# Kernel optimization log

Hardware: AMD Instinct MI355X
Metric: run time of the kernel (lower is better)

The kernel has to match this reference:

```python
import jax, jax.numpy as jnp
import numpy as np

EMBED_DIM = 1024
WINDOW = 256
NUM_HEADS = 16
HEAD_DIM = EMBED_DIM // NUM_HEADS
SCALE = HEAD_DIM ** (-0.5)


def setup_inputs() -> dict:
    key = jax.random.key(0)
    ks = jax.random.split(key, 9)
    B, S, E = 4, 4096, EMBED_DIM
    std = E ** (-0.5)
    x = jax.random.normal(ks[0], (B, S, E), dtype=jnp.float32)
    Wq = jax.random.normal(ks[1], (E, E), dtype=jnp.float32) * std
    Wk = jax.random.normal(ks[2], (E, E), dtype=jnp.float32) * std
    Wv = jax.random.normal(ks[3], (E, E), dtype=jnp.float32) * std
    Wo = jax.random.normal(ks[4], (E, E), dtype=jnp.float32) * std
    bq = jax.random.normal(ks[5], (E,), dtype=jnp.float32) * 0.01
    bk = jax.random.normal(ks[6], (E,), dtype=jnp.float32) * 0.01
    bv = jax.random.normal(ks[7], (E,), dtype=jnp.float32) * 0.01
    bo = jax.random.normal(ks[8], (E,), dtype=jnp.float32) * 0.01
    return {"x": x, "Wq": Wq, "bq": bq, "Wk": Wk, "bk": bk,
            "Wv": Wv, "bv": bv, "Wo": Wo, "bo": bo}


def reference(x, Wq, bq, Wk, bk, Wv, bv, Wo, bo):
    B, S, E = x.shape
    W = WINDOW
    nw = S // W  # seq_len chosen divisible by window_size
    # projections (torch Linear: x @ W.T + b); no head split in the original
    q = x @ Wq.T + bq
    k = x @ Wk.T + bk
    v = x @ Wv.T + bv
    # split into non-overlapping windows: [B, nw, W, E]
    qw = q.reshape(B, nw, W, E)
    kw = k.reshape(B, nw, W, E)
    vw = v.reshape(B, nw, W, E)
    scores = jnp.einsum('bnqe,bnke->bnqk', qw, kw) * SCALE  # [B, nw, W, W]
    causal = jnp.tril(jnp.ones((W, W), dtype=bool))
    scores = jnp.where(causal, scores, -jnp.inf)
    attn = jax.nn.softmax(scores, axis=-1)
    out = jnp.einsum('bnqk,bnke->bnqe', attn, vw).reshape(B, S, E)
    out = out @ Wo.T + bo
    return out + x
```

## Files before the change

kernel.cpp:

```cpp
#include <hip/hip_runtime.h>
#include <hip/hip_bf16.h>


typedef unsigned short u16;
typedef __attribute__((ext_vector_type(8))) short short8;
typedef __attribute__((ext_vector_type(4))) short short4v;
typedef __attribute__((ext_vector_type(4))) float f32x4;

__device__ __forceinline__ u16 f2bf(float f) {
    __hip_bfloat16 h = __float2bfloat16(f);
    return __builtin_bit_cast(u16, h);
}

__device__ __forceinline__ void gl_lds16(const u16* g, u16* l) {
    __builtin_amdgcn_global_load_lds(
        (const __attribute__((address_space(1))) void*)g,
        (__attribute__((address_space(3))) void*)l,
        16, 0, 0);
}

__global__ void prep(const float* __restrict__ x, u16* __restrict__ xb,
                     const float* __restrict__ Wq, const float* __restrict__ Wk,
                     const float* __restrict__ Wv, const float* __restrict__ Wo,
                     u16* __restrict__ WqT, u16* __restrict__ WkT,
                     u16* __restrict__ WvT, u16* __restrict__ Wob,
                     const float* __restrict__ bq, const float* __restrict__ bv,
                     const float* __restrict__ bo,
                     float* __restrict__ u, float* __restrict__ b2)
{
    __shared__ float lt[64][65];
    const int t = threadIdx.x;
    const int blk = blockIdx.x;
    if (blk < 8192) {
        int i = (blk * 256 + t) * 8;
        const float4* s = (const float4*)(x + i);
        float4 a = s[0], b = s[1];
        short8 o;
        o[0] = (short)f2bf(a.x); o[1] = (short)f2bf(a.y); o[2] = (short)f2bf(a.z); o[3] = (short)f2bf(a.w);
        o[4] = (short)f2bf(b.x); o[5] = (short)f2bf(b.y); o[6] = (short)f2bf(b.z); o[7] = (short)f2bf(b.w);
        *(short8*)(xb + i) = o;
        return;
    }
    if (blk < 9216) {
        const int wb = blk - 8192;
        const int which = wb >> 8;
        const int bid = wb & 255;
        const int c0 = (bid & 15) * 64, r0 = (bid >> 4) * 64;
        const int tr = t >> 3, tc = (t & 7) * 8;
        const float* src = which == 0 ? Wq : which == 1 ? Wk : which == 2 ? Wv : Wo;
        if (which == 3) {
#pragma unroll
            for (int p = 0; p < 2; ++p) {
                int r = p * 32 + tr;
                const float* s = src + (size_t)(r0 + r) * 1024 + c0 + tc;
                float4 a = *(const float4*)s, b = *(const float4*)(s + 4);
                short8 o;
                o[0] = (short)f2bf(a.x); o[1] = (short)f2bf(a.y); o[2] = (short)f2bf(a.z); o[3] = (short)f2bf(a.w);
                o[4] = (short)f2bf(b.x); o[5] = (short)f2bf(b.y); o[6] = (short)f2bf(b.z); o[7] = (short)f2bf(b.w);
                *(short8*)(Wob + (size_t)(r0 + r) * 1024 + c0 + tc) = o;
            }
            return;
        }
        u16* dst = which == 0 ? WqT : which == 1 ? WkT : WvT;
#pragma unroll
        for (int p = 0; p < 2; ++p) {
            int r = p * 32 + tr;
            const float* s = src + (size_t)(r0 + r) * 1024 + c0 + tc;
            float4 a = *(const float4*)s, b = *(const float4*)(s + 4);
            lt[r][tc + 0] = a.x; lt[r][tc + 1] = a.y; lt[r][tc + 2] = a.z; lt[r][tc + 3] = a.w;
            lt[r][tc + 4] = b.x; lt[r][tc + 5] = b.y; lt[r][tc + 6] = b.z; lt[r][tc + 7] = b.w;
        }
        __syncthreads();
#pragma unroll
        for (int p = 0; p < 2; ++p) {
            int r = p * 32 + tr;
            short8 o;
#pragma unroll
            for (int j = 0; j < 8; ++j) o[j] = (short)f2bf(lt[tc + j][r]);
            *(short8*)(dst + (size_t)(c0 + r) * 1024 + r0 + tc) = o;
        }
        return;
    }
    {
        const int bid = blk - 9216;
        if (bid < 4) {
            int b = bid * 256 + t;
            float acc = 0.f;
            for (int o = 0; o < 1024; ++o) acc += Wk[(size_t)o * 1024 + b] * bq[o];
            u[b] = acc;
        } else {
            int n = (bid - 4) * 16 + (t >> 4);
            int l = t & 15;
            float acc = 0.f;
            for (int m = l; m < 1024; m += 16) acc += Wo[(size_t)n * 1024 + m] * bv[m];
#pragma unroll
            for (int s = 1; s < 16; s <<= 1) acc += __shfl_xor(acc, s, 64);
            if (l == 0) b2[n] = acc + bo[n];
        }
    }
}

__global__ __launch_bounds__(256, 4) void gemm_small_dual(
    const u16* __restrict__ HA, const u16* __restrict__ HB, u16* __restrict__ HC,
    const u16* __restrict__ WA, const u16* __restrict__ WB, u16* __restrict__ WC)
{
    __shared__ __align__(16) u16 At[64 * 64], Bt[64 * 64];
    const bool sec = blockIdx.x >= 256;
    const u16* A = sec ? WA : HA;
    const u16* B = sec ? WB : HB;
    u16* C = sec ? WC : HC;
    const int bid = blockIdx.x & 255;
    const int m0 = (bid >> 4) * 64, n0 = (bid & 15) * 64;
    const int t = threadIdx.x, lane = t & 63, w = t >> 6;
    const int l15 = lane & 15, lk = lane >> 4;

    f32x4 acc[4];
#pragma unroll
    for (int m = 0; m < 4; ++m) acc[m] = (f32x4){0.f, 0.f, 0.f, 0.f};

    for (int k0 = 0; k0 < 1024; k0 += 64) {
        __syncthreads();
#pragma unroll
        for (int p = 0; p < 2; ++p) {
            int e = p * 2048 + t * 8;
            int row = e >> 6, col = e & 63;
            short8 va = *(const short8*)(A + (size_t)(m0 + row) * 1024 + k0 + col);
            *(short8*)((char*)At + row * 128 + ((col * 2) ^ ((row & 7) << 4))) = va;
            short8 vb = *(const short8*)(B + (size_t)(n0 + row) * 1024 + k0 + col);
            *(short8*)((char*)Bt + row * 128 + ((col * 2) ^ ((row & 7) << 4))) = vb;
        }
        __syncthreads();
#pragma unroll
        for (int ks = 0; ks < 2; ++ks) {
            int bc = ks * 64 + lk * 16;
            int brow = w * 16 + l15;
            short8 bfr = *(const short8*)((char*)Bt + brow * 128 + (bc ^ ((brow & 7) << 4)));
#pragma unroll
            for (int m = 0; m < 4; ++m) {
                int arow = m * 16 + l15;
                short8 af = *(const short8*)((char*)At + arow * 128 + (bc ^ ((arow & 7) << 4)));
                acc[m] = __builtin_amdgcn_mfma_f32_16x16x32_bf16(af, bfr, acc[m], 0, 0, 0);
            }
        }
    }
#pragma unroll
    for (int m = 0; m < 4; ++m)
#pragma unroll
        for (int r = 0; r < 4; ++r) {
            int row = m0 + m * 16 + lk * 4 + r;
            int col = n0 + w * 16 + l15;
            C[(size_t)row * 1024 + col] = f2bf(acc[m][r]);
        }
}

__global__ __launch_bounds__(512) void gemm_yv(
    const u16* __restrict__ A, const u16* __restrict__ BH, const u16* __restrict__ BW,
    const float* __restrict__ ub, u16* __restrict__ Y, u16* __restrict__ V2t)
{
    __shared__ __align__(16) char smbuf[131072];
    char* A0 = smbuf;
    char* B0 = smbuf + 32768;
    char* A1 = smbuf + 65536;
    char* B1 = smbuf + 98304;

    const int t = threadIdx.x;
    const int lane = t & 63, w = t >> 6;
    const int l15 = lane & 15, lk = lane >> 4;
    const int wm = w >> 2, wn = w & 3;
    const int K = 1024;

    const int bid = blockIdx.y * 8 + blockIdx.x;
    const int swz = (bid & 7) * 64 + (bid >> 3);
    const int tn = swz & 7, tm = swz >> 3;
    const int m0 = tm * 256;
    const bool isv = tn >= 4;
    const int n0 = (tn & 3) * 256;
    const u16* B = isv ? BW : BH;

    const int srow = t >> 3;
    const int scg = ((t & 7) ^ (srow & 7)) * 8;

    f32x4 acc[8][4];
#pragma unroll
    for (int mf = 0; mf < 8; ++mf)
#pragma unroll
        for (int nf = 0; nf < 4; ++nf)
            acc[mf][nf] = (f32x4){0.f, 0.f, 0.f, 0.f};

    auto STAGE_T = [&](const u16* G, int gr0, int k0, char* dst) {
#pragma unroll
        for (int h = 0; h < 2; ++h)
#pragma unroll
            for (int c = 0; c < 2; ++c) {
                int ri = h * 128 + c * 64 + srow;
                gl_lds16(G + (size_t)(gr0 + ri) * K + k0 + scg,
                         (u16*)(dst + h * 16384 + c * 8192 + t * 16));
            }
    };
    auto RD = [&](const char* tile, int r, int kc) -> short8 {
        return *(const short8*)(tile + r * 128 + ((kc ^ (r & 7)) << 4));
    };

    short8 av[4], bv[4];
    auto LA = [&](const char* tA, int mfb, int ks) {
#pragma unroll
        for (int f = 0; f < 4; ++f)
            av[f] = RD(tA, wm * 128 + (mfb + f) * 16 + l15, ks * 4 + lk);
    };
    auto LB = [&](const char* tB, int ks) {
#pragma unroll
        for (int f = 0; f < 4; ++f)
            bv[f] = RD(tB, wn * 64 + f * 16 + l15, ks * 4 + lk);
    };
    auto MM = [&](int mfb) {
        __builtin_amdgcn_s_setprio(1);
#pragma unroll
        for (int f = 0; f < 4; ++f)
#pragma unroll
            for (int nf = 0; nf < 4; ++nf)
                acc[mfb + f][nf] = __builtin_amdgcn_mfma_f32_16x16x32_bf16(av[f], bv[nf], acc[mfb + f][nf], 0, 0, 0);
        __builtin_amdgcn_s_setprio(0);
    };
    auto BARW = [&] {
        __builtin_amdgcn_s_barrier();
        asm volatile("s_waitcnt lgkmcnt(0)" ::: "memory");
        __builtin_amdgcn_sched_barrier(0);
    };
    auto BARE = [&] {
        __builtin_amdgcn_s_barrier();
        __builtin_amdgcn_sched_barrier(0);
    };

    STAGE_T(A, m0, 0, A0);
    STAGE_T(B, n0, 0, B0);
    STAGE_T(A, m0, 64, A1);
    STAGE_T(B, n0, 64, B1);
    asm volatile("s_waitcnt vmcnt(8)" ::: "memory");
    __builtin_amdgcn_s_barrier();
    __builtin_amdgcn_sched_barrier(0);

    for (int j = 0; j < 8; ++j) {
        LA(A0, 0, 0); LB(B0, 0);
        if (j >= 1) STAGE_T(A, m0, (2 * j + 1) * 64, A1);
        BARW(); MM(0); BARE();
        LA(A0, 4, 0);
        BARW(); MM(4); BARE();
        LA(A0, 0, 1); LB(B0, 1);
        BARW(); MM(0); BARE();
        LA(A0, 4, 1);
        if (2 * j + 2 < 16) {
            STAGE_T(B, n0, (2 * j + 2) * 64, B0);
            asm volatile("s_waitcnt vmcnt(4)" ::: "memory");
        } else {
            asm volatile("s_waitcnt vmcnt(0)" ::: "memory");
        }
        BARW(); MM(4); BARE();
        LA(A1, 0, 0); LB(B1, 0);
        if (2 * j + 2 < 16) STAGE_T(A, m0, (2 * j + 2) * 64, A0);
        BARW(); MM(0); BARE();
        LA(A1, 4, 0);
        BARW(); MM(4); BARE();
        LA(A1, 0, 1); LB(B1, 1);
        BARW(); MM(0); BARE();
        LA(A1, 4, 1);
        if (2 * j + 3 < 16) {
            STAGE_T(B, n0, (2 * j + 3) * 64, B1);
            asm volatile("s_waitcnt vmcnt(4)" ::: "memory");
        } else {
            asm volatile("s_waitcnt vmcnt(0)" ::: "memory");
        }
        BARW(); MM(4); BARE();
    }

    if (!isv) {
#pragma unroll
        for (int mf = 0; mf < 8; ++mf)
#pragma unroll
            for (int nf = 0; nf < 4; ++nf) {
                int col = n0 + wn * 64 + nf * 16 + l15;
                float bvx = ub[col];
#pragma unroll
                for (int r = 0; r < 4; ++r) {
                    int row = m0 + wm * 128 + mf * 16 + lk * 4 + r;
                    Y[(size_t)row * 1024 + col] = f2bf(acc[mf][nf][r] + bvx);
                }
            }
    } else {
#pragma unroll
        for (int mf = 0; mf < 8; ++mf)
#pragma unroll
            for (int nf = 0; nf < 4; ++nf) {
                int col = n0 + wn * 64 + nf * 16 + l15;
                int row0 = m0 + wm * 128 + mf * 16 + lk * 4;
                short4v pk;
#pragma unroll
                for (int r = 0; r < 4; ++r) pk[r] = (short)f2bf(acc[mf][nf][r]);
                *(short4v*)(V2t + (size_t)col * 16384 + row0) = pk;
            }
    }
}

__global__ __launch_bounds__(256, 1) void attn_win(
    const u16* __restrict__ y, const u16* __restrict__ xb,
    const u16* __restrict__ vt, const float* __restrict__ xres,
    const float* __restrict__ b2, float* __restrict__ outp)
{
    __shared__ __align__(16) char smem[116736];
    u16* P  = (u16*)(smem + 81920);
    float* rmax = (float*)(smem + 114688);
    float* rsum = (float*)(smem + 115712);

    const int t = threadIdx.x;
    const int lane = t & 63, wv = t >> 6;
    const int l15 = lane & 15, lk = lane >> 4;
    const int bid = blockIdx.x;
    const int swz = (bid & 7) * 32 + (bid >> 3);
    const int win = swz >> 2, qc = swz & 3;
    const size_t qrow0 = (size_t)win * 256 + qc * 64;
    const size_t krow0 = (size_t)win * 256;

    f32x4 acc[4][4];
#pragma unroll
    for (int m = 0; m < 4; ++m)
#pragma unroll
        for (int n = 0; n < 4; ++n)
            acc[m][n] = (f32x4){0.f, 0.f, 0.f, 0.f};

    short8 pq[2], pk[8];
    auto LOAD_QK = [&](int e0) {
#pragma unroll
        for (int p = 0; p < 2; ++p) {
            int e = p * 2048 + t * 8;
            pq[p] = *(const short8*)(y + (qrow0 + (e >> 6)) * 1024 + e0 + (e & 63));
        }
#pragma unroll
        for (int p = 0; p < 8; ++p) {
            int e = p * 2048 + t * 8;
            pk[p] = *(const short8*)(xb + (krow0 + (e >> 6)) * 1024 + e0 + (e & 63));
        }
    };
    auto WRITE_QK = [&](int b) {
        char* Qt = smem + b * 40960;
        char* Kt = Qt + 8192;
#pragma unroll
        for (int p = 0; p < 2; ++p) {
            int e = p * 2048 + t * 8;
            int row = e >> 6, col = e & 63;
            *(short8*)(Qt + row * 128 + ((col * 2) ^ ((row & 7) << 4))) = pq[p];
        }
#pragma unroll
        for (int p = 0; p < 8; ++p) {
            int e = p * 2048 + t * 8;
            int row = e >> 6, col = e & 63;
            *(short8*)(Kt + row * 128 + ((col * 2) ^ ((row & 7) << 4))) = pk[p];
        }
    };

    LOAD_QK(0);
    WRITE_QK(0);
    LOAD_QK(64);
    __syncthreads();

    for (int i = 0; i < 16; ++i) {
        const int b = i & 1;
        if (i + 1 < 16) {
            WRITE_QK(b ^ 1);
            if (i + 2 < 16) LOAD_QK((i + 2) * 64);
        }
        const char* Qt = smem + b * 40960;
        const char* Kt = Qt + 8192;
#pragma unroll
        for (int ks = 0; ks < 2; ++ks) {
            const int bc = ks * 64 + lk * 16;
            short8 af[4], bfr[4];
#pragma unroll
            for (int m = 0; m < 4; ++m) {
                int row = m * 16 + l15;
                af[m] = *(const short8*)(Qt + row * 128 + (bc ^ ((row & 7) << 4)));
            }
#pragma unroll
            for (int n = 0; n < 4; ++n) {
                int row = wv * 64 + n * 16 + l15;
                bfr[n] = *(const short8*)(Kt + row * 128 + (bc ^ ((row & 7) << 4)));
            }
            __builtin_amdgcn_s_setprio(1);
#pragma unroll
            for (int m = 0; m < 4; ++m)
#pragma unroll
                for (int n = 0; n < 4; ++n)
                    acc[m][n] = __builtin_amdgcn_mfma_f32_16x16x32_bf16(af[m], bfr[n], acc[m][n], 0, 0, 0);
            __builtin_amdgcn_s_setprio(0);
        }
        __syncthreads();
    }

#pragma unroll
    for (int m = 0; m < 4; ++m)
#pragma unroll
        for (int n = 0; n < 4; ++n) {
            int col = wv * 64 + n * 16 + l15;
#pragma unroll
            for (int r = 0; r < 4; ++r) {
                int qpos = qc * 64 + m * 16 + lk * 4 + r;
                float v = acc[m][n][r] * 0.125f;
                acc[m][n][r] = (col <= qpos) ? v : -1e30f;
            }
        }
#pragma unroll
    for (int m = 0; m < 4; ++m)
#pragma unroll
        for (int r = 0; r < 4; ++r) {
            float tmx = fmaxf(fmaxf(acc[m][0][r], acc[m][1][r]), fmaxf(acc[m][2][r], acc[m][3][r]));
            tmx = fmaxf(tmx, __shfl_xor(tmx, 1));
            tmx = fmaxf(tmx, __shfl_xor(tmx, 2));
            tmx = fmaxf(tmx, __shfl_xor(tmx, 4));
            tmx = fmaxf(tmx, __shfl_xor(tmx, 8));
            if (l15 == 0) rmax[(m * 16 + lk * 4 + r) * 4 + wv] = tmx;
        }
    __syncthreads();
#pragma unroll
    for (int m = 0; m < 4; ++m)
#pragma unroll
        for (int r = 0; r < 4; ++r) {
            int row = m * 16 + lk * 4 + r;
            float m4 = fmaxf(fmaxf(rmax[row * 4], rmax[row * 4 + 1]),
                             fmaxf(rmax[row * 4 + 2], rmax[row * 4 + 3]));
            float s = 0.f;
#pragma unroll
            for (int n = 0; n < 4; ++n) {
                float e = __expf(acc[m][n][r] - m4);
                acc[m][n][r] = e;
                s += e;
            }
            s += __shfl_xor(s, 1);
            s += __shfl_xor(s, 2);
            s += __shfl_xor(s, 4);
            s += __shfl_xor(s, 8);
            if (l15 == 0) rsum[row * 4 + wv] = s;
        }
    __syncthreads();
#pragma unroll
    for (int m = 0; m < 4; ++m)
#pragma unroll
        for (int r = 0; r < 4; ++r) {
            int row = m * 16 + lk * 4 + r;
            float inv = 1.f / (rsum[row * 4] + rsum[row * 4 + 1] + rsum[row * 4 + 2] + rsum[row * 4 + 3]);
#pragma unroll
            for (int n = 0; n < 4; ++n) {
                int col = wv * 64 + n * 16 + l15;
                *(u16*)((char*)P + row * 512 + ((col * 2) ^ ((row & 7) << 4))) = f2bf(acc[m][n][r] * inv);
            }
        }

    short8 pv[8];
    auto LOAD_V = [&](int n0) {
#pragma unroll
        for (int p = 0; p < 8; ++p) {
            int e = p * 2048 + t * 8;
            pv[p] = *(const short8*)(vt + (size_t)(n0 + (e >> 8)) * 16384 + win * 256 + (e & 255));
        }
    };
    auto WRITE_V = [&](int b) {
        char* Vl = smem + b * 40960;
#pragma unroll
        for (int p = 0; p < 8; ++p) {
            int e = p * 2048 + t * 8;
            int row = e >> 8, col = e & 255;
            *(short8*)(Vl + row * 512 + ((col * 2) ^ ((row & 7) << 4))) = pv[p];
        }
    };

    LOAD_V(0);
    WRITE_V(0);
    LOAD_V(64);
    __syncthreads();

    for (int i = 0; i < 16; ++i) {
        const int b = i & 1;
        const int n0 = i * 64;
        if (i + 1 < 16) {
            WRITE_V(b ^ 1);
            if (i + 2 < 16) LOAD_V((i + 2) * 64);
        }
        const char* Vl = smem + b * 40960;
        f32x4 acc2[4];
#pragma unroll
        for (int m = 0; m < 4; ++m) acc2[m] = (f32x4){0.f, 0.f, 0.f, 0.f};
#pragma unroll
        for (int ks = 0; ks < 8; ++ks) {
            const int bc = ks * 64 + lk * 16;
            short8 af[4];
#pragma unroll
            for (int m = 0; m < 4; ++m) {
                int row = m * 16 + l15;
                af[m] = *(const short8*)((char*)P + row * 512 + (bc ^ ((row & 7) << 4)));
            }
            int vrow = wv * 16 + l15;
            short8 bfr = *(const short8*)(Vl + vrow * 512 + (bc ^ ((vrow & 7) << 4)));
            __builtin_amdgcn_s_setprio(1);
#pragma unroll
            for (int m = 0; m < 4; ++m)
                acc2[m] = __builtin_amdgcn_mfma_f32_16x16x32_bf16(af[m], bfr, acc2[m], 0, 0, 0);
            __builtin_amdgcn_s_setprio(0);
        }
#pragma unroll
        for (int m = 0; m < 4; ++m) {
#pragma unroll
            for (int r = 0; r < 4; ++r) {
                int row = m * 16 + lk * 4 + r;
                int col = n0 + wv * 16 + l15;
                size_t idx = (qrow0 + row) * 1024 + col;
                outp[idx] = acc2[m][r] + b2[col] + xres[idx];
            }
        }
        __syncthreads();
    }
}

extern "C" void kernel_launch(void* const* d_in, const int* in_sizes, int n_in,
                              void* d_out, int out_size, void* d_ws, size_t ws_size,
                              hipStream_t stream) {
    const float* x  = (const float*)d_in[0];
    const float* Wq = (const float*)d_in[1];
    const float* bq = (const float*)d_in[2];
    const float* Wk = (const float*)d_in[3];
    const float* Wv = (const float*)d_in[5];
    const float* bv = (const float*)d_in[6];
    const float* Wo = (const float*)d_in[7];
    const float* bo = (const float*)d_in[8];
    float* out = (float*)d_out;

    char* ws = (char*)d_ws;
    u16* xb  = (u16*)(ws);
    u16* yb  = (u16*)(ws + 33554432);
    u16* v2t = (u16*)(ws + 67108864);
    u16* WqT = (u16*)(ws + 100663296);
    u16* WkT = (u16*)(ws + 102760448);
    u16* WvT = (u16*)(ws + 104857600);
    u16* Wob = (u16*)(ws + 106954752);
    u16* Hb  = (u16*)(ws + 109051904);
    u16* W2b = (u16*)(ws + 111149056);
    float* u_  = (float*)(ws + 113246208);
    float* b2_ = (float*)(ws + 113250304);

    prep<<<9284, 256, 0, stream>>>(x, xb, Wq, Wk, Wv, Wo, WqT, WkT, WvT, Wob,
                                   bq, bv, bo, u_, b2_);
    gemm_small_dual<<<512, 256, 0, stream>>>(WkT, WqT, Hb, Wob, WvT, W2b);
    gemm_yv<<<dim3(8, 64), 512, 0, stream>>>(xb, Hb, W2b, u_, yb, v2t);
    attn_win<<<256, 256, 0, stream>>>(yb, xb, v2t, x, b2_, out);
}
```

Measured before the change: 199.4 us.

## Skip causally masked tiles with balanced paired query chunks in window attention

Each block now handles two 32-row query chunks, one early (c) and one late (7-c), so every block does about the same amount of causal work. K/V loads and MFMAs for key tiles that lie fully above the causal diagonal are skipped, and K-tile ownership is interleaved across waves. This is meant to remove the roughly half of QK^T and PV compute and loads that were wasted on masked positions. The cost is extra branching and divergent per-wave work, and the interleaving may leave waves unevenly loaded.

```diff
diff --git a/kernel.cpp b/kernel.cpp
--- a/kernel.cpp
+++ b/kernel.cpp
@@ -315,9 +315,13 @@
     const int l15 = lane & 15, lk = lane >> 4;
     const int bid = blockIdx.x;
     const int swz = (bid & 7) * 32 + (bid >> 3);
-    const int win = swz >> 2, qc = swz & 3;
-    const size_t qrow0 = (size_t)win * 256 + qc * 64;
+    const int win = swz >> 2, c = swz & 3;
+    const size_t qlo = (size_t)win * 256 + c * 32;
+    const size_t qhi = (size_t)win * 256 + (7 - c) * 32;
     const size_t krow0 = (size_t)win * 256;
+    const int kvx = (8 - c) * 32;
+    const int tlo = 2 * (c + 1);
+    const int thi = 2 * (8 - c);
 
     f32x4 acc[4][4];
 #pragma unroll
@@ -331,12 +335,16 @@
 #pragma unroll
         for (int p = 0; p < 2; ++p) {
             int e = p * 2048 + t * 8;
-            pq[p] = *(const short8*)(y + (qrow0 + (e >> 6)) * 1024 + e0 + (e & 63));
+            int r = e >> 6;
+            size_t grow = (r < 32) ? (qlo + r) : (qhi + r - 32);
+            pq[p] = *(const short8*)(y + grow * 1024 + e0 + (e & 63));
         }
 #pragma unroll
         for (int p = 0; p < 8; ++p) {
-            int e = p * 2048 + t * 8;
-            pk[p] = *(const short8*)(xb + (krow0 + (e >> 6)) * 1024 + e0 + (e & 63));
+            if (p * 32 < kvx) {
+                int e = p * 2048 + t * 8;
+                pk[p] = *(const short8*)(xb + (krow0 + (e >> 6)) * 1024 + e0 + (e & 63));
+            }
         }
     };
     auto WRITE_QK = [&](int b) {
@@ -350,9 +358,11 @@
         }
 #pragma unroll
         for (int p = 0; p < 8; ++p) {
-            int e = p * 2048 + t * 8;
-            int row = e >> 6, col = e & 63;
-            *(short8*)(Kt + row * 128 + ((col * 2) ^ ((row & 7) << 4))) = pk[p];
+            if (p * 32 < kvx) {
+                int e = p * 2048 + t * 8;
+                int row = e >> 6, col = e & 63;
+                *(short8*)(Kt + row * 128 + ((col * 2) ^ ((row & 7) << 4))) = pk[p];
+            }
         }
     };
 
@@ -372,23 +382,27 @@
 #pragma unroll
         for (int ks = 0; ks < 2; ++ks) {
             const int bc = ks * 64 + lk * 16;
-            short8 af[4], bfr[4];
+            short8 af[4];
 #pragma unroll
             for (int m = 0; m < 4; ++m) {
                 int row = m * 16 + l15;
                 af[m] = *(const short8*)(Qt + row * 128 + (bc ^ ((row & 7) << 4)));
             }
+            __builtin_amdgcn_s_setprio(1);
 #pragma unroll
             for (int n = 0; n < 4; ++n) {
-                int row = wv * 64 + n * 16 + l15;
-                bfr[n] = *(const short8*)(Kt + row * 128 + (bc ^ ((row & 7) << 4)));
-            }
-            __builtin_amdgcn_s_setprio(1);
-#pragma unroll
-            for (int m = 0; m < 4; ++m)
-#pragma unroll
-                for (int n = 0; n < 4; ++n)
-                    acc[m][n] = __builtin_amdgcn_mfma_f32_16x16x32_bf16(af[m], bfr[n], acc[m][n], 0, 0, 0);
+                int tile = n * 4 + wv;
+                if (tile < thi) {
+                    int row = tile * 16 + l15;
+                    short8 bfr = *(const short8*)(Kt + row * 128 + (bc ^ ((row & 7) << 4)));
+                    acc[2][n] = __builtin_amdgcn_mfma_f32_16x16x32_bf16(af[2], bfr, acc[2][n], 0, 0, 0);
+                    acc[3][n] = __builtin_amdgcn_mfma_f32_16x16x32_bf16(af[3], bfr, acc[3][n], 0, 0, 0);
+                    if (tile < tlo) {
+                        acc[0][n] = __builtin_amdgcn_mfma_f32_16x16x32_bf16(af[0], bfr, acc[0][n], 0, 0, 0);
+                        acc[1][n] = __builtin_amdgcn_mfma_f32_16x16x32_bf16(af[1], bfr, acc[1][n], 0, 0, 0);
+                    }
+                }
+            }
             __builtin_amdgcn_s_setprio(0);
         }
         __syncthreads();
@@ -398,10 +412,11 @@
     for (int m = 0; m < 4; ++m)
 #pragma unroll
         for (int n = 0; n < 4; ++n) {
-            int col = wv * 64 + n * 16 + l15;
+            int col = (n * 4 + wv) * 16 + l15;
 #pragma unroll
             for (int r = 0; r < 4; ++r) {
-                int qpos = qc * 64 + m * 16 + lk * 4 + r;
+                int qpos = (m < 2) ? (c * 32 + m * 16 + lk * 4 + r)
+                                   : ((7 - c) * 32 + (m - 2) * 16 + lk * 4 + r);
                 float v = acc[m][n][r] * 0.125f;
                 acc[m][n][r] = (col <= qpos) ? v : -1e30f;
             }
@@ -447,7 +462,7 @@
             float inv = 1.f / (rsum[row * 4] + rsum[row * 4 + 1] + rsum[row * 4 + 2] + rsum[row * 4 + 3]);
 #pragma unroll
             for (int n = 0; n < 4; ++n) {
-                int col = wv * 64 + n * 16 + l15;
+                int col = (n * 4 + wv) * 16 + l15;
                 *(u16*)((char*)P + row * 512 + ((col * 2) ^ ((row & 7) << 4))) = f2bf(acc[m][n][r] * inv);
             }
         }
@@ -457,7 +472,8 @@
 #pragma unroll
         for (int p = 0; p < 8; ++p) {
             int e = p * 2048 + t * 8;
-            pv[p] = *(const short8*)(vt + (size_t)(n0 + (e >> 8)) * 16384 + win * 256 + (e & 255));
+            if ((e & 255) < kvx)
+                pv[p] = *(const short8*)(vt + (size_t)(n0 + (e >> 8)) * 16384 + win * 256 + (e & 255));
         }
     };
     auto WRITE_V = [&](int b) {
@@ -465,8 +481,10 @@
 #pragma unroll
         for (int p = 0; p < 8; ++p) {
             int e = p * 2048 + t * 8;
-            int row = e >> 8, col = e & 255;
-            *(short8*)(Vl + row * 512 + ((col * 2) ^ ((row & 7) << 4))) = pv[p];
+            if ((e & 255) < kvx) {
+                int row = e >> 8, col = e & 255;
+                *(short8*)(Vl + row * 512 + ((col * 2) ^ ((row & 7) << 4))) = pv[p];
+            }
         }
     };
 
@@ -488,28 +506,34 @@
         for (int m = 0; m < 4; ++m) acc2[m] = (f32x4){0.f, 0.f, 0.f, 0.f};
 #pragma unroll
         for (int ks = 0; ks < 8; ++ks) {
-            const int bc = ks * 64 + lk * 16;
-            short8 af[4];
-#pragma unroll
-            for (int m = 0; m < 4; ++m) {
-                int row = m * 16 + l15;
-                af[m] = *(const short8*)((char*)P + row * 512 + (bc ^ ((row & 7) << 4)));
-            }
-            int vrow = wv * 16 + l15;
-            short8 bfr = *(const short8*)(Vl + vrow * 512 + (bc ^ ((vrow & 7) << 4)));
-            __builtin_amdgcn_s_setprio(1);
-#pragma unroll
-            for (int m = 0; m < 4; ++m)
-                acc2[m] = __builtin_amdgcn_mfma_f32_16x16x32_bf16(af[m], bfr, acc2[m], 0, 0, 0);
-            __builtin_amdgcn_s_setprio(0);
+            if (ks < 8 - c) {
+                const int bc = ks * 64 + lk * 16;
+                short8 af[4];
+#pragma unroll
+                for (int m = 0; m < 4; ++m) {
+                    int row = m * 16 + l15;
+                    af[m] = *(const short8*)((char*)P + row * 512 + (bc ^ ((row & 7) << 4)));
+                }
+                int vrow = wv * 16 + l15;
+                short8 bfr = *(const short8*)(Vl + vrow * 512 + (bc ^ ((vrow & 7) << 4)));
+                __builtin_amdgcn_s_setprio(1);
+                acc2[2] = __builtin_amdgcn_mfma_f32_16x16x32_bf16(af[2], bfr, acc2[2], 0, 0, 0);
+                acc2[3] = __builtin_amdgcn_mfma_f32_16x16x32_bf16(af[3], bfr, acc2[3], 0, 0, 0);
+                if (ks < c + 1) {
+                    acc2[0] = __builtin_amdgcn_mfma_f32_16x16x32_bf16(af[0], bfr, acc2[0], 0, 0, 0);
+                    acc2[1] = __builtin_amdgcn_mfma_f32_16x16x32_bf16(af[1], bfr, acc2[1], 0, 0, 0);
+                }
+                __builtin_amdgcn_s_setprio(0);
+            }
         }
 #pragma unroll
         for (int m = 0; m < 4; ++m) {
 #pragma unroll
             for (int r = 0; r < 4; ++r) {
-                int row = m * 16 + lk * 4 + r;
+                int lrow = (m < 2) ? (m * 16 + lk * 4 + r) : ((m - 2) * 16 + lk * 4 + r);
+                size_t grow = (m < 2) ? (qlo + lrow) : (qhi + lrow);
                 int col = n0 + wv * 16 + l15;
-                size_t idx = (qrow0 + row) * 1024 + col;
+                size_t idx = grow * 1024 + col;
                 outp[idx] = acc2[m][r] + b2[col] + xres[idx];
             }
         }
```

After: 192.2 us. -3.6%, faster.
